# Kernel optimization log

Hardware: AMD Instinct MI355X
Metric: run time of the kernel (lower is better)

## Reference

```python
import math
import jax, jax.numpy as jnp
import numpy as np

IN_DIM = 512
OUT_DIM = 512
K = 3
EPS = 1e-8


def setup_inputs() -> dict:
    key = jax.random.key(0)
    k1, k2, k3 = jax.random.split(key, 3)
    b, h, w = 8, 64, 64
    x = jax.random.normal(k1, (b, IN_DIM, h, w), dtype=jnp.float32)
    style = jax.random.normal(k2, (b, IN_DIM), dtype=jnp.float32)
    weight = jax.random.normal(k3, (OUT_DIM, IN_DIM, K, K), dtype=jnp.float32)
    bias = jnp.zeros((OUT_DIM,), dtype=jnp.float32)
    return {"x": x, "style": style, "weight": weight, "bias": bias}


def _mod_weights(weight, style):
    # EqualizedWeight scaling: c = 1/sqrt(prod(shape[1:]))
    c = 1.0 / math.sqrt(IN_DIM * K * K)
    w = weight * c                                    # [out, in, k, k]
    ws = w[None] * (style[:, None, :, None, None] + 1.0)  # [b, out, in, k, k]
    sigma_inv = jax.lax.rsqrt(jnp.sum(ws * ws, axis=(2, 3, 4), keepdims=True) + EPS)
    return ws * sigma_inv


def reference(x, style, weight, bias):
    ws = _mod_weights(weight, style)                  # [b, out, in, k, k]

    def conv_one(xi, wi):
        # xi: [in, h, w], wi: [out, in, k, k]
        y = jax.lax.conv_general_dilated(
            xi[None], wi, window_strides=(1, 1), padding="SAME",
            dimension_numbers=("NCHW", "OIHW", "NCHW"))
        return y[0]

    out = jax.vmap(conv_one)(x, ws)                   # [b, out, h, w]
    return out + bias[None, :, None, None]
```

## Files before the change

kernel.cpp:

```cpp
#include <hip/hip_runtime.h>

#define CIN 512
#define COUT 512
#define HH 64
#define WW 64
#define BB 8
#define KTOT 4608

#define XPD 66
#define NSL 66
#define BUFSH (6 * NSL * 64)

typedef __attribute__((ext_vector_type(8))) short short8;
typedef __attribute__((ext_vector_type(4))) float f32x4;

__device__ inline unsigned short f2bf(float f) {
    unsigned int u = __float_as_uint(f);
    u += 0x7FFFu + ((u >> 16) & 1u);
    return (unsigned short)(u >> 16);
}

__device__ inline void gll16(const void* g, void* l) {
    __builtin_amdgcn_global_load_lds(
        (const __attribute__((address_space(1))) unsigned int*)g,
        (__attribute__((address_space(3))) unsigned int*)l, 16, 0, 0);
}

__global__ __launch_bounds__(256) void zring_kernel(unsigned short* __restrict__ xtp) {
    const int e = blockIdx.x * 256 + threadIdx.x;
    if (e >= BB * 260 * 64) return;
    const int unit = e & 63;
    const int sa = e >> 6;
    const int b = sa / 260;
    const int s = sa - b * 260;
    int yy, xx;
    if (s < 66)       { yy = 0;        xx = s; }
    else if (s < 132) { yy = 65;       xx = s - 66; }
    else if (s < 196) { yy = s - 131;  xx = 0; }
    else              { yy = s - 195;  xx = 65; }
    *(short8*)(xtp + ((size_t)(b * XPD + yy) * XPD + xx) * 512 + unit * 8) =
        (short8){0, 0, 0, 0, 0, 0, 0, 0};
}

__global__ __launch_bounds__(256) void xpose_kernel(const float* __restrict__ x,
                                                    const float* __restrict__ style,
                                                    unsigned short* __restrict__ xtp) {
    __shared__ float tile[32 * 65];
    __shared__ float sst[32];
    const int ic = blockIdx.x;
    const int y  = blockIdx.y;
    const int b  = blockIdx.z;
    const int t  = threadIdx.x;
    if (t < 32) sst[t] = style[b * CIN + ic * 32 + t] + 1.0f;
#pragma unroll
    for (int it = 0; it < 8; ++it) {
        int e = it * 256 + t;
        int ii = e >> 6, xx = e & 63;
        tile[ii * 65 + xx] = x[(((size_t)(b * CIN + ic * 32 + ii) * HH + y) << 6) + xx];
    }
    __syncthreads();
#pragma unroll
    for (int it = 0; it < 8; ++it) {
        int g = it * 256 + t;
        int xx = g >> 5, ii = g & 31;
        xtp[((size_t)(b * XPD + y + 1) * XPD + xx + 1) * 512 + ic * 32 + ii] =
            f2bf(tile[ii * 65 + xx] * sst[ii]);
    }
}

__global__ __launch_bounds__(256) void wpack_kernel(const float* __restrict__ weight,
                                                    unsigned short* __restrict__ wpk) {
    __shared__ float q[KTOT];
    const int o = blockIdx.x;
    const int t = threadIdx.x;
    const float* wrow = weight + (size_t)o * KTOT;
    const float cst = 1.0f / sqrtf((float)KTOT);
#pragma unroll
    for (int it = 0; it < 18; ++it) {
        int e = it * 256 + t;
        q[e] = wrow[e] * cst;
    }
    __syncthreads();
    const int g = o >> 4, l15 = o & 15;
    for (int m = t; m < 576; m += 256) {
        int c   = m / 36;
        int rem = m - c * 36;
        int tap = rem >> 2;
        int l4  = rem & 3;
        short8 v;
#pragma unroll
        for (int e = 0; e < 8; ++e)
            v[e] = (short)f2bf(q[(c * 32 + l4 * 8 + e) * 9 + tap]);
        *(short8*)(wpk + ((((size_t)c * 9 + tap) * 32 + g) * 64 + l4 * 16 + l15) * 8) = v;
    }
}

__global__ __launch_bounds__(256) void sigma_kernel(const float* __restrict__ weight,
                                                    const float* __restrict__ style,
                                                    float* __restrict__ siginv) {
    __shared__ float sred[4][8];
    const int o = blockIdx.x;
    const int t = threadIdx.x;
    const float* wrow = weight + (size_t)o * KTOT;
    float acc[8] = {0.f, 0.f, 0.f, 0.f, 0.f, 0.f, 0.f, 0.f};
#pragma unroll
    for (int ii = 0; ii < 2; ++ii) {
        const int i = t * 2 + ii;
        float wsq = 0.f;
#pragma unroll
        for (int tap = 0; tap < 9; ++tap) {
            float v = wrow[i * 9 + tap];
            wsq += v * v;
        }
#pragma unroll
        for (int b = 0; b < 8; ++b) {
            float s = style[b * CIN + i] + 1.0f;
            acc[b] += wsq * s * s;
        }
    }
#pragma unroll
    for (int b = 0; b < 8; ++b) {
        float v = acc[b];
#pragma unroll
        for (int off = 32; off > 0; off >>= 1) v += __shfl_down(v, off, 64);
        if ((t & 63) == 0) sred[t >> 6][b] = v;
    }
    __syncthreads();
    if (t < 8) {
        const float S = sred[0][t] + sred[1][t] + sred[2][t] + sred[3][t];
        siginv[t * COUT + o] = rsqrtf(S * (1.0f / (float)KTOT) + 1e-8f);
    }
}

__global__ __launch_bounds__(512, 2) void conv_kernel(const unsigned short* __restrict__ wpk,
                                                      const unsigned short* __restrict__ xtp,
                                                      const float* __restrict__ siginv,
                                                      const float* __restrict__ bias,
                                                      float* __restrict__ out) {
    __shared__ __align__(16) unsigned short xs[2 * BUFSH];
    const int bid = blockIdx.x;
    const int k  = bid & 7;
    const int tq = bid >> 3;
    const int ob = k & 1;
    const int b  = (k >> 1) * 2 + (tq >> 4);
    const int yb = tq & 15;

    const int tid  = threadIdx.x;
    const int lane = tid & 63;
    const int wid_u = __builtin_amdgcn_readfirstlane(tid >> 6);
    const int l15 = lane & 15, l4 = lane >> 4;
    const int l8  = lane & 7,  lq = lane >> 3;
    const int og = wid_u & 1, rp = wid_u >> 1;
    const int y0 = yb * 4;
    const int g0 = ob * 16 + og * 8;

    int vB[3][2];
#pragma unroll
    for (int kx = 0; kx < 3; ++kx)
#pragma unroll
        for (int ks = 0; ks < 2; ++ks)
            vB[kx][ks] = (l15 + kx) * 128 + (((ks * 4 + l4) ^ ((l15 + kx) & 7)) * 16);

    f32x4 acc[8][4];
#pragma unroll
    for (int mi = 0; mi < 8; ++mi)
#pragma unroll
        for (int j = 0; j < 4; ++j) acc[mi][j] = (f32x4){0.f, 0.f, 0.f, 0.f};

    short8 af[3][8];

#define STAGE(bufp, icq)                                                                  \
    do {                                                                                  \
        for (int qq = wid_u; qq < 54; qq += 8) {                                          \
            const int ir  = qq / 9;                                                       \
            const int sub = qq - ir * 9;                                                  \
            const int yin = y0 - 1 + ir;                                                  \
            const unsigned short* srow = xtp + (size_t)(b * XPD + yin + 1) * XPD * 512;   \
            if (sub < 8) {                                                                \
                const int xcol = sub * 8 + lq;                                            \
                gll16(srow + (size_t)xcol * 512 + (icq) * 64 + (l8 ^ lq) * 8,             \
                      xs + (bufp) * BUFSH + (ir * NSL + sub * 8) * 64);                   \
            } else if (lane < 16) {                                                       \
                const int xcol = 64 + lq;                                                 \
                gll16(srow + (size_t)xcol * 512 + (icq) * 64 + (l8 ^ lq) * 8,             \
                      xs + (bufp) * BUFSH + (ir * NSL + 64) * 64);                        \
            }                                                                             \
        }                                                                                 \
    } while (0)

#define LOAD_SET(slot, icv, s)                                                            \
    do {                                                                                  \
        const unsigned short* ab = wpk +                                                  \
            ((size_t)(((icv) * 2 + ((s) & 1)) * 9 + ((s) >> 1)) * 32 + g0) * 512;         \
        _Pragma("unroll") for (int mi = 0; mi < 8; ++mi)                                  \
            af[slot][mi] = *(const short8*)(ab + mi * 512 + lane * 8);                    \
    } while (0)

#define COMPUTE(slot, ky, kx, ks, cbase)                                                  \
    do {                                                                                  \
        short8 bfr[4];                                                                    \
        const char* bp = (const char*)xs + (cbase) + (rp + (ky)) * (NSL * 128) +          \
                         vB[kx][ks];                                                      \
        _Pragma("unroll") for (int j = 0; j < 4; ++j)                                     \
            bfr[j] = *(const short8*)(bp + j * 2048);                                     \
        __builtin_amdgcn_s_setprio(1);                                                    \
        _Pragma("unroll") for (int mi = 0; mi < 8; ++mi)                                  \
            _Pragma("unroll") for (int j = 0; j < 4; ++j)                                 \
                acc[mi][j] = __builtin_amdgcn_mfma_f32_16x16x32_bf16(                     \
                    af[slot][mi], bfr[j], acc[mi][j], 0, 0, 0);                           \
        __builtin_amdgcn_s_setprio(0);                                                    \
    } while (0)

    STAGE(0, 0);
    LOAD_SET(0, 0, 0);
    LOAD_SET(1, 0, 1);
    __syncthreads();

#pragma unroll 1
    for (int ic = 0; ic < 8; ++ic) {
        if (ic < 7) STAGE((ic + 1) & 1, ic + 1);
        const int cbase = (ic & 1) * (BUFSH * 2);
#pragma unroll
        for (int s = 0; s < 18; ++s) {
            if (s < 16) { LOAD_SET((s + 2) % 3, ic, s + 2); }
            else        { LOAD_SET((s + 2) % 3, ic + 1, s - 16); }
            COMPUTE(s % 3, (s >> 1) / 3, (s >> 1) % 3, s & 1, cbase);
        }
        __syncthreads();
    }

    const int yout = y0 + rp;
#pragma unroll
    for (int mi = 0; mi < 8; ++mi) {
        const int obase = ob * 256 + og * 128 + mi * 16 + l4 * 4;
#pragma unroll
        for (int rr = 0; rr < 4; ++rr) {
            const int o = obase + rr;
            const float sv = siginv[b * COUT + o];
            const float bv = bias[o];
            float* orow = out + (((size_t)(b * COUT + o) * HH + yout) << 6);
#pragma unroll
            for (int j = 0; j < 4; ++j) {
                orow[j * 16 + l15] = acc[mi][j][rr] * sv + bv;
            }
        }
    }
#undef STAGE
#undef LOAD_SET
#undef COMPUTE
}

extern "C" void kernel_launch(void* const* d_in, const int* in_sizes, int n_in,
                              void* d_out, int out_size, void* d_ws, size_t ws_size,
                              hipStream_t stream) {
    const float* x      = (const float*)d_in[0];
    const float* style  = (const float*)d_in[1];
    const float* weight = (const float*)d_in[2];
    const float* bias   = (const float*)d_in[3];
    float* out = (float*)d_out;

    unsigned short* wpk = (unsigned short*)d_ws;
    unsigned short* xtp = wpk + (size_t)2359296;
    float* siginv = (float*)(xtp + (size_t)BB * XPD * XPD * 512);

    zring_kernel<<<520, 256, 0, stream>>>(xtp);
    xpose_kernel<<<dim3(16, HH, BB), 256, 0, stream>>>(x, style, xtp);
    wpack_kernel<<<COUT, 256, 0, stream>>>(weight, wpk);
    sigma_kernel<<<COUT, 256, 0, stream>>>(weight, style, siginv);
    conv_kernel<<<256, 512, 0, stream>>>(wpk, xtp, siginv, bias, out);
}
```

Measured before the change: 166.1 us.

## Shrink conv tile to 2 rows and 32-channel chunks, double occupancy

The implicit-GEMM conv tile is restructured. Each block now covers 2 output rows instead of 4, with 4 output-channel groups of 64 per wave, and input channels are staged in 16 chunks of 32 rather than 8 chunks of 64. The grid doubles to 512 blocks and launch bounds ask for 4 blocks per CU. The software-pipelined weight register prefetch across taps is replaced by direct per-tap loads, and the LDS swizzle and staging addressing are rewritten. The aim is more resident waves and better latency hiding, at the cost of less reuse of each weight fragment, more syncs per block and more redundant halo loads.

```diff
diff --git a/kernel.cpp b/kernel.cpp
--- a/kernel.cpp
+++ b/kernel.cpp
@@ -8,8 +8,8 @@
 #define KTOT 4608
 
 #define XPD 66
-#define NSL 66
-#define BUFSH (6 * NSL * 64)
+#define BUFSH (4 * 66 * 32)
+#define ROWB (66 * 64)
 
 typedef __attribute__((ext_vector_type(8))) short short8;
 typedef __attribute__((ext_vector_type(4))) float f32x4;
@@ -132,7 +132,7 @@
     }
 }
 
-__global__ __launch_bounds__(512, 2) void conv_kernel(const unsigned short* __restrict__ wpk,
+__global__ __launch_bounds__(512, 4) void conv_kernel(const unsigned short* __restrict__ wpk,
                                                       const unsigned short* __restrict__ xtp,
                                                       const float* __restrict__ siginv,
                                                       const float* __restrict__ bias,
@@ -142,97 +142,89 @@
     const int k  = bid & 7;
     const int tq = bid >> 3;
     const int ob = k & 1;
-    const int b  = (k >> 1) * 2 + (tq >> 4);
-    const int yb = tq & 15;
+    const int b  = (k >> 1) * 2 + (tq >> 5);
+    const int yb = tq & 31;
+    const int y0 = yb * 2;
 
     const int tid  = threadIdx.x;
     const int lane = tid & 63;
     const int wid_u = __builtin_amdgcn_readfirstlane(tid >> 6);
     const int l15 = lane & 15, l4 = lane >> 4;
-    const int l8  = lane & 7,  lq = lane >> 3;
-    const int og = wid_u & 1, rp = wid_u >> 1;
-    const int y0 = yb * 4;
-    const int g0 = ob * 16 + og * 8;
-
-    int vB[3][2];
+    const int og = wid_u & 3, rp = wid_u >> 2;
+    const int g0 = ob * 16 + og * 4;
+
+    const int u = lane & 3;
+    const int sl0 = wid_u * 16 + (lane >> 2);
+    const int row0 = sl0 / 66, col0 = sl0 - row0 * 66;
+    const int sl1 = sl0 + 128;
+    const int row1 = sl1 / 66, col1 = sl1 - row1 * 66;
+    const int col2 = 58 + (lane >> 2);
+    const unsigned short* src0 =
+        xtp + ((size_t)(b * XPD + y0 + row0) * XPD + col0) * 512 + (u ^ (col0 & 3)) * 8;
+    const unsigned short* src1 =
+        xtp + ((size_t)(b * XPD + y0 + row1) * XPD + col1) * 512 + (u ^ (col1 & 3)) * 8;
+    const unsigned short* src2 =
+        xtp + ((size_t)(b * XPD + y0 + 3) * XPD + col2) * 512 + (u ^ (col2 & 3)) * 8;
+
+    int vB[3];
 #pragma unroll
     for (int kx = 0; kx < 3; ++kx)
-#pragma unroll
-        for (int ks = 0; ks < 2; ++ks)
-            vB[kx][ks] = (l15 + kx) * 128 + (((ks * 4 + l4) ^ ((l15 + kx) & 7)) * 16);
-
-    f32x4 acc[8][4];
-#pragma unroll
-    for (int mi = 0; mi < 8; ++mi)
+        vB[kx] = (l15 + kx) * 64 + ((l4 ^ ((l15 + kx) & 3)) * 16);
+
+    f32x4 acc[4][4];
+#pragma unroll
+    for (int mi = 0; mi < 4; ++mi)
 #pragma unroll
         for (int j = 0; j < 4; ++j) acc[mi][j] = (f32x4){0.f, 0.f, 0.f, 0.f};
 
-    short8 af[3][8];
+    const unsigned short* wB = wpk + (size_t)g0 * 512 + lane * 8;
 
 #define STAGE(bufp, icq)                                                                  \
     do {                                                                                  \
-        for (int qq = wid_u; qq < 54; qq += 8) {                                          \
-            const int ir  = qq / 9;                                                       \
-            const int sub = qq - ir * 9;                                                  \
-            const int yin = y0 - 1 + ir;                                                  \
-            const unsigned short* srow = xtp + (size_t)(b * XPD + yin + 1) * XPD * 512;   \
-            if (sub < 8) {                                                                \
-                const int xcol = sub * 8 + lq;                                            \
-                gll16(srow + (size_t)xcol * 512 + (icq) * 64 + (l8 ^ lq) * 8,             \
-                      xs + (bufp) * BUFSH + (ir * NSL + sub * 8) * 64);                   \
-            } else if (lane < 16) {                                                       \
-                const int xcol = 64 + lq;                                                 \
-                gll16(srow + (size_t)xcol * 512 + (icq) * 64 + (l8 ^ lq) * 8,             \
-                      xs + (bufp) * BUFSH + (ir * NSL + 64) * 64);                        \
-            }                                                                             \
-        }                                                                                 \
+        unsigned short* dbase = xs + (bufp) * BUFSH + wid_u * 512;                        \
+        gll16(src0 + (size_t)(icq) * 32, dbase);                                          \
+        gll16(src1 + (size_t)(icq) * 32, dbase + 4096);                                   \
+        if (wid_u == 0 && lane < 32)                                                      \
+            gll16(src2 + (size_t)(icq) * 32, xs + (bufp) * BUFSH + 8192);                 \
     } while (0)
 
-#define LOAD_SET(slot, icv, s)                                                            \
+#define PHASE(tap, wAc, cbase)                                                            \
     do {                                                                                  \
-        const unsigned short* ab = wpk +                                                  \
-            ((size_t)(((icv) * 2 + ((s) & 1)) * 9 + ((s) >> 1)) * 32 + g0) * 512;         \
-        _Pragma("unroll") for (int mi = 0; mi < 8; ++mi)                                  \
-            af[slot][mi] = *(const short8*)(ab + mi * 512 + lane * 8);                    \
-    } while (0)
-
-#define COMPUTE(slot, ky, kx, ks, cbase)                                                  \
-    do {                                                                                  \
+        short8 afx[4];                                                                    \
+        _Pragma("unroll") for (int mi = 0; mi < 4; ++mi)                                  \
+            afx[mi] = *(const short8*)((wAc) + (tap) * 16384 + mi * 512);                 \
         short8 bfr[4];                                                                    \
-        const char* bp = (const char*)xs + (cbase) + (rp + (ky)) * (NSL * 128) +          \
-                         vB[kx][ks];                                                      \
+        const char* bp = (const char*)xs + (cbase) +                                      \
+                         (rp + (tap) / 3) * ROWB + vB[(tap) % 3];                         \
         _Pragma("unroll") for (int j = 0; j < 4; ++j)                                     \
-            bfr[j] = *(const short8*)(bp + j * 2048);                                     \
+            bfr[j] = *(const short8*)(bp + j * 1024);                                     \
         __builtin_amdgcn_s_setprio(1);                                                    \
-        _Pragma("unroll") for (int mi = 0; mi < 8; ++mi)                                  \
+        _Pragma("unroll") for (int mi = 0; mi < 4; ++mi)                                  \
             _Pragma("unroll") for (int j = 0; j < 4; ++j)                                 \
                 acc[mi][j] = __builtin_amdgcn_mfma_f32_16x16x32_bf16(                     \
-                    af[slot][mi], bfr[j], acc[mi][j], 0, 0, 0);                           \
+                    afx[mi], bfr[j], acc[mi][j], 0, 0, 0);                                \
         __builtin_amdgcn_s_setprio(0);                                                    \
     } while (0)
 
     STAGE(0, 0);
-    LOAD_SET(0, 0, 0);
-    LOAD_SET(1, 0, 1);
     __syncthreads();
 
 #pragma unroll 1
-    for (int ic = 0; ic < 8; ++ic) {
-        if (ic < 7) STAGE((ic + 1) & 1, ic + 1);
+    for (int ic = 0; ic < 16; ++ic) {
+        if (ic < 15) STAGE((ic + 1) & 1, ic + 1);
+        const unsigned short* wAc = wB + (size_t)ic * (9 * 32 * 512);
         const int cbase = (ic & 1) * (BUFSH * 2);
 #pragma unroll
-        for (int s = 0; s < 18; ++s) {
-            if (s < 16) { LOAD_SET((s + 2) % 3, ic, s + 2); }
-            else        { LOAD_SET((s + 2) % 3, ic + 1, s - 16); }
-            COMPUTE(s % 3, (s >> 1) / 3, (s >> 1) % 3, s & 1, cbase);
+        for (int tap = 0; tap < 9; ++tap) {
+            PHASE(tap, wAc, cbase);
         }
         __syncthreads();
     }
 
     const int yout = y0 + rp;
 #pragma unroll
-    for (int mi = 0; mi < 8; ++mi) {
-        const int obase = ob * 256 + og * 128 + mi * 16 + l4 * 4;
+    for (int mi = 0; mi < 4; ++mi) {
+        const int obase = ob * 256 + og * 64 + mi * 16 + l4 * 4;
 #pragma unroll
         for (int rr = 0; rr < 4; ++rr) {
             const int o = obase + rr;
@@ -246,8 +238,7 @@
         }
     }
 #undef STAGE
-#undef LOAD_SET
-#undef COMPUTE
+#undef PHASE
 }
 
 extern "C" void kernel_launch(void* const* d_in, const int* in_sizes, int n_in,
@@ -267,5 +258,5 @@
     xpose_kernel<<<dim3(16, HH, BB), 256, 0, stream>>>(x, style, xtp);
     wpack_kernel<<<COUT, 256, 0, stream>>>(weight, wpk);
     sigma_kernel<<<COUT, 256, 0, stream>>>(weight, style, siginv);
-    conv_kernel<<<256, 512, 0, stream>>>(wpk, xtp, siginv, bias, out);
-}
+    conv_kernel<<<512, 512, 0, stream>>>(wpk, xtp, siginv, bias, out);
+}
```

Result: no change. 167.2 us (+0.6%).
